# Kernel tuning notes

Hardware: AMD Instinct MI355X
Metric: run time of the kernel (lower is better)

The kernel has to match this reference:

```python
import jax, jax.numpy as jnp
from jax import lax
import numpy as np

# ViT-Base/16 config (matches module defaults)
IMG, P, NC = 224, 16, 2
D, DEPTH, H, MLP = 768, 12, 12, 3072
DK = D // H
NPATCH = (IMG // P) ** 2          # 196
N = NPATCH + 1                    # 197 tokens incl. cls
B = 32


def _ln(x, w, b, eps=1e-5):
    mu = jnp.mean(x, axis=-1, keepdims=True)
    var = jnp.mean((x - mu) ** 2, axis=-1, keepdims=True)
    return (x - mu) * lax.rsqrt(var + eps) * w + b


def _gelu(x):
    # torch nn.GELU default = exact erf formulation
    return jax.nn.gelu(x, approximate=False)


def setup_inputs() -> dict:
    key = jax.random.key(0)
    ks = iter(jax.random.split(key, 32))
    std = 0.02
    d = {
        "x": jax.random.normal(next(ks), (B, 3, IMG, IMG), jnp.float32),
        "conv_w": jax.random.normal(next(ks), (D, 3, P, P), jnp.float32) * std,
        "conv_b": jnp.zeros((D,), jnp.float32),
        "cls_token": jax.random.normal(next(ks), (1, 1, D), jnp.float32) * std,
        "pos_embed": jax.random.normal(next(ks), (1, N, D), jnp.float32) * std,
        # stacked per-block params, leading dim = DEPTH; Linear weights stored [in, out]
        "ln1_w": jnp.ones((DEPTH, D), jnp.float32),
        "ln1_b": jnp.zeros((DEPTH, D), jnp.float32),
        "wq": jax.random.normal(next(ks), (DEPTH, D, D), jnp.float32) * std,
        "wk": jax.random.normal(next(ks), (DEPTH, D, D), jnp.float32) * std,
        "wv": jax.random.normal(next(ks), (DEPTH, D, D), jnp.float32) * std,
        "wo_w": jax.random.normal(next(ks), (DEPTH, D, D), jnp.float32) * std,
        "wo_b": jnp.zeros((DEPTH, D), jnp.float32),
        "ln2_w": jnp.ones((DEPTH, D), jnp.float32),
        "ln2_b": jnp.zeros((DEPTH, D), jnp.float32),
        "mlp1_w": jax.random.normal(next(ks), (DEPTH, D, MLP), jnp.float32) * std,
        "mlp1_b": jnp.zeros((DEPTH, MLP), jnp.float32),
        "mlp2_w": jax.random.normal(next(ks), (DEPTH, MLP, D), jnp.float32) * std,
        "mlp2_b": jnp.zeros((DEPTH, D), jnp.float32),
        "fnorm_w": jnp.ones((D,), jnp.float32),
        "fnorm_b": jnp.zeros((D,), jnp.float32),
        "hln_w": jnp.ones((D,), jnp.float32),
        "hln_b": jnp.zeros((D,), jnp.float32),
        "h1_w": jax.random.normal(next(ks), (D, MLP), jnp.float32) * std,
        "h1_b": jnp.zeros((MLP,), jnp.float32),
        "h2_w": jax.random.normal(next(ks), (MLP, NC), jnp.float32) * std,
        "h2_b": jnp.zeros((NC,), jnp.float32),
    }
    return d


def reference(x, conv_w, conv_b, cls_token, pos_embed, ln1_w, ln1_b, wq, wk, wv,
              wo_w, wo_b, ln2_w, ln2_b, mlp1_w, mlp1_b, mlp2_w, mlp2_b,
              fnorm_w, fnorm_b, hln_w, hln_b, h1_w, h1_b, h2_w, h2_b):
    b = x.shape[0]
    # patch embed: conv stride=patch + GELU (dropout is inference no-op)
    p = lax.conv_general_dilated(x, conv_w, (P, P), 'VALID',
                                 dimension_numbers=('NCHW', 'OIHW', 'NCHW'))
    p = _gelu(p + conv_b[None, :, None, None])        # [B, D, 14, 14]
    tok = p.reshape(b, D, NPATCH).transpose(0, 2, 1)  # [B, 196, D]
    tok = jnp.concatenate([jnp.broadcast_to(cls_token, (b, 1, D)), tok], axis=1)
    tok = tok + pos_embed                              # [B, N, D]

    scale = DK ** -0.5
    for i in range(DEPTH):
        h = _ln(tok, ln1_w[i], ln1_b[i])
        q = (h @ wq[i]).reshape(b, N, H, DK)
        k = (h @ wk[i]).reshape(b, N, H, DK)
        v = (h @ wv[i]).reshape(b, N, H, DK)
        scores = jnp.einsum('bnhd,bmhd->bhnm', q, k) * scale
        attn = jax.nn.softmax(scores, axis=-1)
        ctx = jnp.einsum('bhnm,bmhd->bnhd', attn, v).reshape(b, N, D)
        tok = tok + (ctx @ wo_w[i] + wo_b[i])
        h = _ln(tok, ln2_w[i], ln2_b[i])
        tok = tok + (_gelu(h @ mlp1_w[i] + mlp1_b[i]) @ mlp2_w[i] + mlp2_b[i])

    tok = _ln(tok, fnorm_w, fnorm_b)
    cls = _ln(tok[:, 0], hln_w, hln_b)
    logits = _gelu(cls @ h1_w + h1_b) @ h2_w + h2_b    # [B, 2]
    return logits
```

## Files before the change

### kernel.cpp

```cpp
#include <hip/hip_runtime.h>
#include <hip/hip_bf16.h>
#include <stdint.h>

#define L_DEPTH 12
#define DM      768
#define NHEAD   12
#define DK      64
#define DMLP    3072
#define BB      32
#define NTOK    197
#define NPATCH  196
#define MTOK    (BB*NTOK)
#define MPAD    6400
#define MPE     (BB*NPATCH)

typedef __attribute__((ext_vector_type(8))) short short8;
typedef __attribute__((ext_vector_type(4))) float f4;

#define AS1C(p) ((const __attribute__((address_space(1))) void*)(p))
#define AS3(p)  ((__attribute__((address_space(3))) void*)(p))

__device__ __forceinline__ float bf2f(unsigned short u) {
    union { float f; unsigned int i; } v; v.i = ((unsigned int)u) << 16; return v.f;
}
__device__ __forceinline__ unsigned short f2bf(float f) {
    union { float f; unsigned int i; } v; v.f = f;
    unsigned int i = v.i;
    i += 0x7fffu + ((i >> 16) & 1u);
    return (unsigned short)(i >> 16);
}
__device__ __forceinline__ float gelu_f(float x) {
    return 0.5f * x * (1.0f + erff(x * 0.7071067811865475f));
}

__global__ void cvt_bf16(const float* __restrict__ src, unsigned short* __restrict__ dst, int n) {
    int i = blockIdx.x * 256 + threadIdx.x;
    if (i < n) dst[i] = f2bf(src[i]);
}

__global__ void tconv(const float* __restrict__ src, unsigned short* __restrict__ dst,
                      int K, int Nsrc, int row_off, int Ntot) {
    const int l = blockIdx.z;
    src += (size_t)l * K * Nsrc;
    dst += (size_t)l * Ntot * K + (size_t)row_off * K;
    __shared__ float t[32][33];
    const int tid = threadIdx.x;
    const int tx = tid & 31, ty = tid >> 5;
    const int n0 = blockIdx.x * 32, k0 = blockIdx.y * 32;
#pragma unroll
    for (int u = 0; u < 4; ++u) {
        int k = k0 + ty + u * 8;
        t[ty + u * 8][tx] = src[(size_t)k * Nsrc + n0 + tx];
    }
    __syncthreads();
#pragma unroll
    for (int u = 0; u < 4; ++u) {
        int n = n0 + ty + u * 8;
        dst[(size_t)n * K + k0 + tx] = f2bf(t[tx][ty + u * 8]);
    }
}

__global__ void im2col_k(const float* __restrict__ x, unsigned short* __restrict__ A) {
    int idx = blockIdx.x * 256 + threadIdx.x;
    int k = idx % DM, row = idx / DM;
    int b = row / NPATCH, p = row % NPATCH;
    int py = p / 14, px = p % 14;
    int c = k >> 8, rem = k & 255, i = rem >> 4, j = rem & 15;
    float v = x[(((size_t)b * 3 + c) * 224 + py * 16 + i) * 224 + px * 16 + j];
    A[idx] = f2bf(v);
}

__global__ void assemble_tok(const float* __restrict__ pe, const float* __restrict__ cls_t,
                             const float* __restrict__ pos, float* __restrict__ tok) {
    int idx = blockIdx.x * 256 + threadIdx.x;
    int d = idx % DM, row = idx / DM;
    int b = row / NTOK, n = row % NTOK;
    float v = (n == 0) ? cls_t[d] : pe[((size_t)b * NPATCH + n - 1) * DM + d];
    tok[idx] = v + pos[(size_t)n * DM + d];
}

template <int EPI>
__global__ __launch_bounds__(256, 2)
void gemm128(const unsigned short* __restrict__ A, const unsigned short* __restrict__ Bt,
             const float* __restrict__ bias, const float* res,
             void* Cout, int M, int N, int K) {
    __shared__ __align__(16) unsigned short As[128 * 32];
    __shared__ __align__(16) unsigned short Bs[128 * 32];
    const int tid = threadIdx.x;
    const int lane = tid & 63, wave = tid >> 6;
    const int wm = wave >> 1, wn = wave & 1;
    const int lr = lane & 15, quad = lane >> 4;

    const int L = blockIdx.y * gridDim.x + blockIdx.x;
    const int xcd = L & 7, pos = L >> 3;
    const int by = xcd + 8 * (pos / gridDim.x);
    const int bx = pos % gridDim.x;
    const int bm = by * 128, bn = bx * 128;
    if (bm >= M) return;

    f4 acc[4][4];
#pragma unroll
    for (int i = 0; i < 4; ++i)
#pragma unroll
        for (int j = 0; j < 4; ++j) acc[i][j] = (f4){0.f, 0.f, 0.f, 0.f};

    for (int k0 = 0; k0 < K; k0 += 32) {
#pragma unroll
        for (int u = 0; u < 2; ++u) {
            int c = tid + u * 256;
            int row = c >> 2, kc = c & 3;
            __builtin_amdgcn_global_load_lds(
                AS1C(A + (size_t)(bm + row) * K + k0 + kc * 8),
                AS3(&As[(wave * 64 + u * 256) * 8]), 16, 0, 0);
            __builtin_amdgcn_global_load_lds(
                AS1C(Bt + (size_t)(bn + row) * K + k0 + kc * 8),
                AS3(&Bs[(wave * 64 + u * 256) * 8]), 16, 0, 0);
        }
        __syncthreads();
        short8 af[4], bfr[4];
#pragma unroll
        for (int i = 0; i < 4; ++i)
            af[i] = *(const short8*)&As[(wm * 64 + i * 16 + lr) * 32 + quad * 8];
#pragma unroll
        for (int j = 0; j < 4; ++j)
            bfr[j] = *(const short8*)&Bs[(wn * 64 + j * 16 + lr) * 32 + quad * 8];
#pragma unroll
        for (int i = 0; i < 4; ++i)
#pragma unroll
            for (int j = 0; j < 4; ++j)
                acc[i][j] = __builtin_amdgcn_mfma_f32_16x16x32_bf16(af[i], bfr[j], acc[i][j], 0, 0, 0);
        __syncthreads();
    }

#pragma unroll
    for (int i = 0; i < 4; ++i)
#pragma unroll
        for (int j = 0; j < 4; ++j)
#pragma unroll
            for (int r = 0; r < 4; ++r) {
                int row = bm + wm * 64 + i * 16 + quad * 4 + r;
                int col = bn + wn * 64 + j * 16 + lr;
                float v = acc[i][j][r];
                if (EPI == 1 || EPI == 2 || EPI == 3) v += bias[col];
                if (EPI == 1 || EPI == 3) v = gelu_f(v);
                if (EPI == 2) v += res[(size_t)row * N + col];
                if (EPI == 0 || EPI == 1)
                    ((unsigned short*)Cout)[(size_t)row * N + col] = f2bf(v);
                else
                    ((float*)Cout)[(size_t)row * N + col] = v;
            }
}

__global__ __launch_bounds__(256)
void ln_bf16(const float* __restrict__ x, const float* __restrict__ w,
             const float* __restrict__ b, unsigned short* __restrict__ out) {
    __shared__ float red[8];
    const int tid = threadIdx.x;
    const size_t row = blockIdx.x;
    const float* xr = x + row * DM;
    float v0 = xr[tid], v1 = xr[tid + 256], v2 = xr[tid + 512];
    float s = v0 + v1 + v2, s2 = v0 * v0 + v1 * v1 + v2 * v2;
    for (int o = 32; o > 0; o >>= 1) { s += __shfl_down(s, o); s2 += __shfl_down(s2, o); }
    if ((tid & 63) == 0) { red[(tid >> 6) * 2] = s; red[(tid >> 6) * 2 + 1] = s2; }
    __syncthreads();
    s = red[0] + red[2] + red[4] + red[6];
    s2 = red[1] + red[3] + red[5] + red[7];
    float mean = s * (1.f / DM);
    float rstd = rsqrtf(s2 * (1.f / DM) - mean * mean + 1e-5f);
    out[row * DM + tid]       = f2bf((v0 - mean) * rstd * w[tid]       + b[tid]);
    out[row * DM + tid + 256] = f2bf((v1 - mean) * rstd * w[tid + 256] + b[tid + 256]);
    out[row * DM + tid + 512] = f2bf((v2 - mean) * rstd * w[tid + 512] + b[tid + 512]);
}

#define ASTR 72
#define VSTR 232
#define MP   208

__global__ __launch_bounds__(256)
void attn_fused(const unsigned short* __restrict__ qkv, unsigned short* __restrict__ ctx) {
    __shared__ __align__(16) unsigned short Qs[MP * ASTR];
    __shared__ __align__(16) unsigned short Ks[MP * ASTR];
    __shared__ __align__(16) unsigned short Vt[64 * VSTR];
    __shared__ __align__(16) unsigned short Ps[4][16 * VSTR];
    const int tid = threadIdx.x;
    const int lane = tid & 63, wave = tid >> 6;
    const int lr = lane & 15, quad = lane >> 4;
    const int bh = blockIdx.x;
    const int b = bh / NHEAD, h = bh % NHEAD;
    const size_t rowbase = (size_t)b * NTOK * 2304 + (size_t)h * 64;

    for (int e = tid; e < 64 * (224 - NTOK); e += 256) {
        int r = e / (224 - NTOK), c = NTOK + e % (224 - NTOK);
        Vt[r * VSTR + c] = 0;
    }
    for (int e = tid; e < 64 * 16; e += 256) {
        int r = e >> 4, c = MP + (e & 15);
        ((unsigned short*)Ps)[r * VSTR + c] = 0;
    }
    const short8 z8 = {0, 0, 0, 0, 0, 0, 0, 0};
    for (int c = tid; c < MP * 8; c += 256) {
        int row = c >> 3, d0 = (c & 7) * 8;
        short8 q = z8, k = z8;
        if (row < NTOK) {
            const size_t g = rowbase + (size_t)row * 2304 + d0;
            q = *(const short8*)(qkv + g);
            k = *(const short8*)(qkv + g + 768);
        }
        *(short8*)&Qs[row * ASTR + d0] = q;
        *(short8*)&Ks[row * ASTR + d0] = k;
    }
    for (int c = tid; c < NTOK * 8; c += 256) {
        int m = c >> 3, d0 = (c & 7) * 8;
        short8 v = *(const short8*)(qkv + rowbase + 1536 + (size_t)m * 2304 + d0);
#pragma unroll
        for (int u = 0; u < 8; ++u) Vt[(d0 + u) * VSTR + m] = v[u];
    }
    __syncthreads();

    for (int it = 0; it < 4; ++it) {
        const int strip = wave + it * 4;
        const bool valid = strip < 13;
        float invl[4];
        if (valid) {
            const int n0 = strip * 16;
            const short8 a0 = *(const short8*)&Qs[(n0 + lr) * ASTR + quad * 8];
            const short8 a1 = *(const short8*)&Qs[(n0 + lr) * ASTR + 32 + quad * 8];
            f4 acc[13];
#pragma unroll
            for (int t = 0; t < 13; ++t) acc[t] = (f4){0.f, 0.f, 0.f, 0.f};
#pragma unroll
            for (int t = 0; t < 13; ++t) {
                short8 b0 = *(const short8*)&Ks[(t * 16 + lr) * ASTR + quad * 8];
                short8 b1 = *(const short8*)&Ks[(t * 16 + lr) * ASTR + 32 + quad * 8];
                acc[t] = __builtin_amdgcn_mfma_f32_16x16x32_bf16(a0, b0, acc[t], 0, 0, 0);
                acc[t] = __builtin_amdgcn_mfma_f32_16x16x32_bf16(a1, b1, acc[t], 0, 0, 0);
            }
            float mx[4] = {-3e38f, -3e38f, -3e38f, -3e38f};
#pragma unroll
            for (int t = 0; t < 13; ++t) {
                bool maskc = (t == 12) && (lr >= 5);
#pragma unroll
                for (int rr = 0; rr < 4; ++rr) {
                    float v = maskc ? -3e38f : acc[t][rr] * 0.125f;
                    acc[t][rr] = v;
                    mx[rr] = fmaxf(mx[rr], v);
                }
            }
#pragma unroll
            for (int rr = 0; rr < 4; ++rr) {
                mx[rr] = fmaxf(mx[rr], __shfl_xor(mx[rr], 1, 16));
                mx[rr] = fmaxf(mx[rr], __shfl_xor(mx[rr], 2, 16));
                mx[rr] = fmaxf(mx[rr], __shfl_xor(mx[rr], 4, 16));
                mx[rr] = fmaxf(mx[rr], __shfl_xor(mx[rr], 8, 16));
            }
            float sm[4] = {0.f, 0.f, 0.f, 0.f};
#pragma unroll
            for (int t = 0; t < 13; ++t)
#pragma unroll
                for (int rr = 0; rr < 4; ++rr) {
                    float pv = __expf(acc[t][rr] - mx[rr]);
                    acc[t][rr] = pv;
                    sm[rr] += pv;
                }
#pragma unroll
            for (int rr = 0; rr < 4; ++rr) {
                sm[rr] += __shfl_xor(sm[rr], 1, 16);
                sm[rr] += __shfl_xor(sm[rr], 2, 16);
                sm[rr] += __shfl_xor(sm[rr], 4, 16);
                sm[rr] += __shfl_xor(sm[rr], 8, 16);
                invl[rr] = 1.f / sm[rr];
            }
            unsigned short* pw = &Ps[wave][0];
#pragma unroll
            for (int t = 0; t < 13; ++t)
#pragma unroll
                for (int rr = 0; rr < 4; ++rr)
                    pw[(quad * 4 + rr) * VSTR + t * 16 + lr] = f2bf(acc[t][rr]);
        }
        __syncthreads();
        if (valid) {
            f4 accc[4];
#pragma unroll
            for (int t = 0; t < 4; ++t) accc[t] = (f4){0.f, 0.f, 0.f, 0.f};
#pragma unroll
            for (int s = 0; s < 7; ++s) {
                short8 pa = *(const short8*)&Ps[wave][lr * VSTR + s * 32 + quad * 8];
#pragma unroll
                for (int t = 0; t < 4; ++t) {
                    short8 vb = *(const short8*)&Vt[(t * 16 + lr) * VSTR + s * 32 + quad * 8];
                    accc[t] = __builtin_amdgcn_mfma_f32_16x16x32_bf16(pa, vb, accc[t], 0, 0, 0);
                }
            }
            const int n0 = strip * 16;
#pragma unroll
            for (int t = 0; t < 4; ++t)
#pragma unroll
                for (int rr = 0; rr < 4; ++rr) {
                    int n = n0 + quad * 4 + rr;
                    if (n < NTOK)
                        ctx[((size_t)(b * NTOK + n)) * DM + h * 64 + t * 16 + lr] =
                            f2bf(accc[t][rr] * invl[rr]);
                }
        }
        __syncthreads();
    }
}

__global__ __launch_bounds__(256)
void head_ln(const float* __restrict__ tok, const float* __restrict__ fw, const float* __restrict__ fb,
             const float* __restrict__ hw, const float* __restrict__ hb, float* __restrict__ cls) {
    __shared__ float red[8];
    const int tid = threadIdx.x;
    const float* xr = tok + (size_t)blockIdx.x * NTOK * DM;
    float v0 = xr[tid], v1 = xr[tid + 256], v2 = xr[tid + 512];
    float s = v0 + v1 + v2, s2 = v0 * v0 + v1 * v1 + v2 * v2;
    for (int o = 32; o > 0; o >>= 1) { s += __shfl_down(s, o); s2 += __shfl_down(s2, o); }
    if ((tid & 63) == 0) { red[(tid >> 6) * 2] = s; red[(tid >> 6) * 2 + 1] = s2; }
    __syncthreads();
    s = red[0] + red[2] + red[4] + red[6];
    s2 = red[1] + red[3] + red[5] + red[7];
    float mean = s * (1.f / DM), rstd = rsqrtf(s2 * (1.f / DM) - mean * mean + 1e-5f);
    v0 = (v0 - mean) * rstd * fw[tid]       + fb[tid];
    v1 = (v1 - mean) * rstd * fw[tid + 256] + fb[tid + 256];
    v2 = (v2 - mean) * rstd * fw[tid + 512] + fb[tid + 512];
    __syncthreads();
    s = v0 + v1 + v2; s2 = v0 * v0 + v1 * v1 + v2 * v2;
    for (int o = 32; o > 0; o >>= 1) { s += __shfl_down(s, o); s2 += __shfl_down(s2, o); }
    if ((tid & 63) == 0) { red[(tid >> 6) * 2] = s; red[(tid >> 6) * 2 + 1] = s2; }
    __syncthreads();
    s = red[0] + red[2] + red[4] + red[6];
    s2 = red[1] + red[3] + red[5] + red[7];
    mean = s * (1.f / DM); rstd = rsqrtf(s2 * (1.f / DM) - mean * mean + 1e-5f);
    float* cr = cls + (size_t)blockIdx.x * DM;
    cr[tid]       = (v0 - mean) * rstd * hw[tid]       + hb[tid];
    cr[tid + 256] = (v1 - mean) * rstd * hw[tid + 256] + hb[tid + 256];
    cr[tid + 512] = (v2 - mean) * rstd * hw[tid + 512] + hb[tid + 512];
}

__global__ __launch_bounds__(256)
void head_mlp1(const float* __restrict__ cls, const float* __restrict__ w,
               const float* __restrict__ bias, float* __restrict__ outv) {
    __shared__ float cl[DM];
    const int tid = threadIdx.x;
    const int b = blockIdx.y;
    const int col = blockIdx.x * 256 + tid;
    for (int e = tid; e < DM; e += 256) cl[e] = cls[(size_t)b * DM + e];
    __syncthreads();
    float s = bias[col];
    for (int k = 0; k < DM; ++k) s += cl[k] * w[(size_t)k * DMLP + col];
    outv[(size_t)b * DMLP + col] = gelu_f(s);
}

__global__ __launch_bounds__(256)
void head_mlp2(const float* __restrict__ midh, const float* __restrict__ w,
               const float* __restrict__ bias, float* __restrict__ out) {
    __shared__ float red[256];
    const int tid = threadIdx.x;
    const int b = blockIdx.x >> 1, c = blockIdx.x & 1;
    float s = 0.f;
    for (int k = tid; k < DMLP; k += 256) s += midh[(size_t)b * DMLP + k] * w[(size_t)k * 2 + c];
    red[tid] = s;
    __syncthreads();
    for (int o = 128; o > 0; o >>= 1) { if (tid < o) red[tid] += red[tid + o]; __syncthreads(); }
    if (tid == 0) out[blockIdx.x] = red[0] + bias[c];
}

extern "C" void kernel_launch(void* const* d_in, const int* in_sizes, int n_in,
                              void* d_out, int out_size, void* d_ws, size_t ws_size,
                              hipStream_t stream) {
    if (n_in < 26) return;
    const float* x       = (const float*)d_in[0];
    const float* conv_w  = (const float*)d_in[1];
    const float* conv_b  = (const float*)d_in[2];
    const float* cls_tok = (const float*)d_in[3];
    const float* pos     = (const float*)d_in[4];
    const float* ln1_w   = (const float*)d_in[5];
    const float* ln1_b   = (const float*)d_in[6];
    const float* wq      = (const float*)d_in[7];
    const float* wk      = (const float*)d_in[8];
    const float* wv      = (const float*)d_in[9];
    const float* wo_w    = (const float*)d_in[10];
    const float* wo_b    = (const float*)d_in[11];
    const float* ln2_w   = (const float*)d_in[12];
    const float* ln2_b   = (const float*)d_in[13];
    const float* mlp1_w  = (const float*)d_in[14];
    const float* mlp1_b  = (const float*)d_in[15];
    const float* mlp2_w  = (const float*)d_in[16];
    const float* mlp2_b  = (const float*)d_in[17];
    const float* fnorm_w = (const float*)d_in[18];
    const float* fnorm_b = (const float*)d_in[19];
    const float* hln_w   = (const float*)d_in[20];
    const float* hln_b   = (const float*)d_in[21];
    const float* h1_w    = (const float*)d_in[22];
    const float* h1_b    = (const float*)d_in[23];
    const float* h2_w    = (const float*)d_in[24];
    const float* h2_b    = (const float*)d_in[25];

    char* p = (char*)d_ws;
    auto alloc = [&](size_t bytes) -> char* {
        char* r = p; p += (bytes + 255) & ~(size_t)255; return r;
    };
    unsigned short* Wqkv = (unsigned short*)alloc((size_t)L_DEPTH * 2304 * 768 * 2);
    unsigned short* Wo   = (unsigned short*)alloc((size_t)L_DEPTH * 768 * 768 * 2);
    unsigned short* Wm1  = (unsigned short*)alloc((size_t)L_DEPTH * 3072 * 768 * 2);
    unsigned short* Wm2  = (unsigned short*)alloc((size_t)L_DEPTH * 768 * 3072 * 2);
    unsigned short* CW   = (unsigned short*)alloc((size_t)768 * 768 * 2);
    unsigned short* AIM  = (unsigned short*)alloc((size_t)MPE * 768 * 2);
    float*          PE   = (float*)alloc((size_t)MPE * 768 * 4);
    float*          TOK  = (float*)alloc((size_t)MPAD * 768 * 4);
    unsigned short* HB   = (unsigned short*)alloc((size_t)MPAD * 768 * 2);
    unsigned short* QKV  = (unsigned short*)alloc((size_t)MPAD * 2304 * 2);
    unsigned short* CTX  = (unsigned short*)alloc((size_t)MPAD * 768 * 2);
    unsigned short* MID  = (unsigned short*)alloc((size_t)MPAD * 3072 * 2);
    float*          CLS  = (float*)alloc((size_t)BB * 768 * 4);
    float*          MDH  = (float*)alloc((size_t)BB * 3072 * 4);
    if ((size_t)(p - (char*)d_ws) > ws_size) return;

    tconv<<<dim3(24, 24, L_DEPTH), 256, 0, stream>>>(wq, Wqkv, 768, 768, 0,    2304);
    tconv<<<dim3(24, 24, L_DEPTH), 256, 0, stream>>>(wk, Wqkv, 768, 768, 768,  2304);
    tconv<<<dim3(24, 24, L_DEPTH), 256, 0, stream>>>(wv, Wqkv, 768, 768, 1536, 2304);
    tconv<<<dim3(24, 24, L_DEPTH), 256, 0, stream>>>(wo_w, Wo, 768, 768, 0, 768);
    tconv<<<dim3(96, 24, L_DEPTH), 256, 0, stream>>>(mlp1_w, Wm1, 768, 3072, 0, 3072);
    tconv<<<dim3(24, 96, L_DEPTH), 256, 0, stream>>>(mlp2_w, Wm2, 3072, 768, 0, 768);
    cvt_bf16<<<2304, 256, 0, stream>>>(conv_w, CW, 768 * 768);

    const int NYP = 56;

    im2col_k<<<(MPE * 768) / 256, 256, 0, stream>>>(x, AIM);
    gemm128<3><<<dim3(6, NYP), 256, 0, stream>>>(AIM, CW, conv_b, nullptr, PE, MPE, 768, 768);
    assemble_tok<<<(MTOK * 768) / 256, 256, 0, stream>>>(PE, cls_tok, pos, TOK);

    for (int l = 0; l < L_DEPTH; ++l) {
        ln_bf16<<<MTOK, 256, 0, stream>>>(TOK, ln1_w + (size_t)l * 768, ln1_b + (size_t)l * 768, HB);
        gemm128<0><<<dim3(18, NYP), 256, 0, stream>>>(
            HB, Wqkv + (size_t)l * 2304 * 768, nullptr, nullptr, QKV, MPAD, 2304, 768);
        attn_fused<<<BB * NHEAD, 256, 0, stream>>>(QKV, CTX);
        gemm128<2><<<dim3(6, NYP), 256, 0, stream>>>(
            CTX, Wo + (size_t)l * 768 * 768, wo_b + (size_t)l * 768, TOK, TOK, MPAD, 768, 768);
        ln_bf16<<<MTOK, 256, 0, stream>>>(TOK, ln2_w + (size_t)l * 768, ln2_b + (size_t)l * 768, HB);
        gemm128<1><<<dim3(24, NYP), 256, 0, stream>>>(
            HB, Wm1 + (size_t)l * 3072 * 768, mlp1_b + (size_t)l * 3072, nullptr, MID, MPAD, 3072, 768);
        gemm128<2><<<dim3(6, NYP), 256, 0, stream>>>(
            MID, Wm2 + (size_t)l * 768 * 3072, mlp2_b + (size_t)l * 768, TOK, TOK, MPAD, 768, 3072);
    }

    head_ln<<<BB, 256, 0, stream>>>(TOK, fnorm_w, fnorm_b, hln_w, hln_b, CLS);
    head_mlp1<<<dim3(12, BB), 256, 0, stream>>>(CLS, h1_w, h1_b, MDH);
    head_mlp2<<<BB * 2, 256, 0, stream>>>(MDH, h2_w, h2_b, (float*)d_out);
}
```

Measured before the change: 3.800 ms.

## Double-buffer LDS tiles in gemm128 to overlap global loads with MFMA

The GEMM main loop now keeps two LDS buffers for A and B tiles and issues async global-to-LDS loads for the next K-slice before computing on the current one, leaving one barrier per iteration instead of two. Per-thread source pointers are also hoisted out of the loop. This aims to hide global memory latency behind the MFMA work, at the cost of doubling LDS use per block, which could reduce occupancy. Correctness depends on how the compiler places the vmcnt waits before the barrier.

```diff
diff --git a/kernel.cpp b/kernel.cpp
--- a/kernel.cpp
+++ b/kernel.cpp
@@ -84,8 +84,8 @@
 void gemm128(const unsigned short* __restrict__ A, const unsigned short* __restrict__ Bt,
              const float* __restrict__ bias, const float* res,
              void* Cout, int M, int N, int K) {
-    __shared__ __align__(16) unsigned short As[128 * 32];
-    __shared__ __align__(16) unsigned short Bs[128 * 32];
+    __shared__ __align__(16) unsigned short As[2][128 * 32];
+    __shared__ __align__(16) unsigned short Bs[2][128 * 32];
     const int tid = threadIdx.x;
     const int lane = tid & 63, wave = tid >> 6;
     const int wm = wave >> 1, wn = wave & 1;
@@ -104,32 +104,40 @@
 #pragma unroll
         for (int j = 0; j < 4; ++j) acc[i][j] = (f4){0.f, 0.f, 0.f, 0.f};
 
-    for (int k0 = 0; k0 < K; k0 += 32) {
-#pragma unroll
-        for (int u = 0; u < 2; ++u) {
-            int c = tid + u * 256;
-            int row = c >> 2, kc = c & 3;
-            __builtin_amdgcn_global_load_lds(
-                AS1C(A + (size_t)(bm + row) * K + k0 + kc * 8),
-                AS3(&As[(wave * 64 + u * 256) * 8]), 16, 0, 0);
-            __builtin_amdgcn_global_load_lds(
-                AS1C(Bt + (size_t)(bn + row) * K + k0 + kc * 8),
-                AS3(&Bs[(wave * 64 + u * 256) * 8]), 16, 0, 0);
-        }
-        __syncthreads();
+    const int c0 = tid, c1 = tid + 256;
+    const int row0 = c0 >> 2, kc0 = c0 & 3;
+    const int row1 = c1 >> 2, kc1 = c1 & 3;
+    const unsigned short* a0p = A + (size_t)(bm + row0) * K + kc0 * 8;
+    const unsigned short* a1p = A + (size_t)(bm + row1) * K + kc1 * 8;
+    const unsigned short* b0p = Bt + (size_t)(bn + row0) * K + kc0 * 8;
+    const unsigned short* b1p = Bt + (size_t)(bn + row1) * K + kc1 * 8;
+
+    auto stage = [&](int k0, int buf) {
+        __builtin_amdgcn_global_load_lds(AS1C(a0p + k0), AS3(&As[buf][(wave * 64) * 8]), 16, 0, 0);
+        __builtin_amdgcn_global_load_lds(AS1C(b0p + k0), AS3(&Bs[buf][(wave * 64) * 8]), 16, 0, 0);
+        __builtin_amdgcn_global_load_lds(AS1C(a1p + k0), AS3(&As[buf][(wave * 64 + 256) * 8]), 16, 0, 0);
+        __builtin_amdgcn_global_load_lds(AS1C(b1p + k0), AS3(&Bs[buf][(wave * 64 + 256) * 8]), 16, 0, 0);
+    };
+
+    stage(0, 0);
+    __syncthreads();
+    const int nk = K >> 5;
+    for (int ki = 0; ki < nk; ++ki) {
+        const int cur = ki & 1;
+        if (ki + 1 < nk) stage((ki + 1) * 32, cur ^ 1);
         short8 af[4], bfr[4];
 #pragma unroll
         for (int i = 0; i < 4; ++i)
-            af[i] = *(const short8*)&As[(wm * 64 + i * 16 + lr) * 32 + quad * 8];
+            af[i] = *(const short8*)&As[cur][(wm * 64 + i * 16 + lr) * 32 + quad * 8];
 #pragma unroll
         for (int j = 0; j < 4; ++j)
-            bfr[j] = *(const short8*)&Bs[(wn * 64 + j * 16 + lr) * 32 + quad * 8];
+            bfr[j] = *(const short8*)&Bs[cur][(wn * 64 + j * 16 + lr) * 32 + quad * 8];
 #pragma unroll
         for (int i = 0; i < 4; ++i)
 #pragma unroll
             for (int j = 0; j < 4; ++j)
                 acc[i][j] = __builtin_amdgcn_mfma_f32_16x16x32_bf16(af[i], bfr[j], acc[i][j], 0, 0, 0);
-        __syncthreads();
+        if (ki + 1 < nk) __syncthreads();
     }
 
 #pragma unroll
```

After: 3.804 ms. Within noise of the previous version (+0.1%).
